# Kernel optimization log

Measured on AMD Instinct MI355X. Metric: run time of the kernel, lower is better.

Reference implementation:

```python
import jax, jax.numpy as jnp
import numpy as np

B, E, K = 512, 4096, 1024      # batch, emb_dim, key_dim
M, L = 1024, 32                # mem_size, prompt_length
TOP_K = 4
EPS = 1e-12


def _l2norm(x, axis=-1):
    n = jnp.linalg.norm(x, axis=axis, keepdims=True)
    return x / jnp.maximum(n, EPS)


def setup_inputs() -> dict:
    key = jax.random.key(0)
    k1, k2, k3, k4 = jax.random.split(key, 4)
    return {
        "x_query": jax.random.normal(k1, (B, E), dtype=jnp.float32),
        "W_proj": jax.random.normal(k2, (K, E), dtype=jnp.float32) * 0.02,
        "prompt_memory": jax.random.normal(k3, (M, L, E), dtype=jnp.float32) * 0.02,
        "prompt_keys": jax.random.normal(k4, (M, K), dtype=jnp.float32) * 0.02,
        "top_k": TOP_K,
    }


def reference(x_query, W_proj, prompt_memory, prompt_keys, top_k):
    # x_proj = Linear(emb_dim -> key_dim, no bias): x @ W.T
    x_proj = jnp.einsum("be,ke->bk", x_query, W_proj)          # [B, K]
    x_norm = _l2norm(x_proj)                                     # [B, K]
    key_norm = _l2norm(prompt_keys)                              # [M, K]
    sim = jnp.einsum("bk,mk->bm", x_norm, key_norm)             # [B, M]
    _, idx = jax.lax.top_k(sim, top_k)                           # [B, top_k]
    sel_prompts = prompt_memory[idx]                             # [B, top_k, L, E]
    sel_keys = _l2norm(prompt_keys[idx], axis=2)                 # [B, top_k, K]
    refined = jnp.einsum("bk,btk->bt", x_norm, sel_keys)        # [B, top_k]
    w = jax.nn.softmax(refined, axis=1)                          # [B, top_k]
    # softmax-weighted sum over selected prompts
    out = jnp.einsum("btle,bt->ble", sel_prompts, w)            # [B, L, E]
    return out
```

## Files before the change

kernel.cpp:

```cpp
#include <hip/hip_runtime.h>
#include <math.h>

#define BDIM 512
#define EDIM 4096
#define KDIM 1024
#define MDIM 1024
#define LDIM 32
#define TOPK 4
#define EPSF 1e-12f

typedef __attribute__((ext_vector_type(8))) short short8;
typedef __attribute__((ext_vector_type(4))) float f32x4;

struct us4 { ushort x, y, z, w; };

__device__ inline ushort f2bf_rn(float x) {
    union { float f; unsigned u; } v; v.f = x;
    unsigned r = (v.u + 0x7FFF + ((v.u >> 16) & 1)) >> 16;
    return (ushort)r;
}
__device__ inline float bf2f(ushort h) {
    union { unsigned u; float f; } v; v.u = ((unsigned)h) << 16;
    return v.f;
}

__global__ __launch_bounds__(256)
void split_all_kernel(const float* __restrict__ xq, const float* __restrict__ wp,
                      const float* __restrict__ pk,
                      ushort* __restrict__ xq_h, ushort* __restrict__ xq_l,
                      ushort* __restrict__ wp_h, ushort* __restrict__ wp_l,
                      ushort* __restrict__ pk_h, ushort* __restrict__ pk_l)
{
    const int blk = blockIdx.x;
    const float* src; ushort* hi; ushort* lo; int base;
    if (blk < 512)       { src = xq; hi = xq_h; lo = xq_l; base = blk * 1024; }
    else if (blk < 1536) { src = wp; hi = wp_h; lo = wp_l; base = (blk - 512) * 1024; }
    else                 { src = pk; hi = pk_h; lo = pk_l; base = (blk - 1536) * 1024; }

    #pragma unroll
    for (int it = 0; it < 4; ++it) {
        const int i = base + it * 256 + threadIdx.x;
        float4 v = ((const float4*)src)[i];
        us4 h, l;
        h.x = f2bf_rn(v.x); l.x = f2bf_rn(v.x - bf2f(h.x));
        h.y = f2bf_rn(v.y); l.y = f2bf_rn(v.y - bf2f(h.y));
        h.z = f2bf_rn(v.z); l.z = f2bf_rn(v.z - bf2f(h.z));
        h.w = f2bf_rn(v.w); l.w = f2bf_rn(v.w - bf2f(h.w));
        ((us4*)hi)[i] = h;
        ((us4*)lo)[i] = l;
    }
}

__global__ __launch_bounds__(256)
void gemm_mfma_split(const ushort* __restrict__ Ah, const ushort* __restrict__ Al,
                     const ushort* __restrict__ Bh, const ushort* __restrict__ Bl,
                     float* __restrict__ Cp, int M, int N, int K, int Kchunk)
{
    __shared__ ushort lds[4][64][40];

    const int t  = threadIdx.x;
    const int bn = blockIdx.x, bm = blockIdx.y, kz = blockIdx.z;

    const int srow = t >> 2, sg = t & 3;
    const size_t aoff = (size_t)(bm * 64 + srow) * K + sg * 8 + (size_t)kz * Kchunk;
    const size_t boff = (size_t)(bn * 64 + srow) * K + sg * 8 + (size_t)kz * Kchunk;

    const int lane = t & 63, wid = t >> 6;
    const int wr = wid >> 1, wc = wid & 1;
    const int fr = lane & 15, fg = lane >> 4;

    f32x4 acc[2][2];
    #pragma unroll
    for (int i = 0; i < 2; ++i)
        #pragma unroll
        for (int j = 0; j < 2; ++j)
            acc[i][j] = (f32x4){0.f, 0.f, 0.f, 0.f};

    for (int k0 = 0; k0 < Kchunk; k0 += 32) {
        *(short8*)(&lds[0][srow][sg * 8]) = *(const short8*)(Ah + aoff + k0);
        *(short8*)(&lds[1][srow][sg * 8]) = *(const short8*)(Al + aoff + k0);
        *(short8*)(&lds[2][srow][sg * 8]) = *(const short8*)(Bh + boff + k0);
        *(short8*)(&lds[3][srow][sg * 8]) = *(const short8*)(Bl + boff + k0);
        __syncthreads();

        short8 ah[2], al[2], bh[2], bl[2];
        #pragma unroll
        for (int i = 0; i < 2; ++i) {
            ah[i] = *(const short8*)(&lds[0][wr * 32 + i * 16 + fr][fg * 8]);
            al[i] = *(const short8*)(&lds[1][wr * 32 + i * 16 + fr][fg * 8]);
            bh[i] = *(const short8*)(&lds[2][wc * 32 + i * 16 + fr][fg * 8]);
            bl[i] = *(const short8*)(&lds[3][wc * 32 + i * 16 + fr][fg * 8]);
        }
        #pragma unroll
        for (int i = 0; i < 2; ++i)
            #pragma unroll
            for (int j = 0; j < 2; ++j) {
                acc[i][j] = __builtin_amdgcn_mfma_f32_16x16x32_bf16(ah[i], bh[j], acc[i][j], 0, 0, 0);
                acc[i][j] = __builtin_amdgcn_mfma_f32_16x16x32_bf16(ah[i], bl[j], acc[i][j], 0, 0, 0);
                acc[i][j] = __builtin_amdgcn_mfma_f32_16x16x32_bf16(al[i], bh[j], acc[i][j], 0, 0, 0);
            }
        __syncthreads();
    }

    float* Cz = Cp + (size_t)kz * M * N;
    #pragma unroll
    for (int i = 0; i < 2; ++i)
        #pragma unroll
        for (int j = 0; j < 2; ++j)
            #pragma unroll
            for (int q = 0; q < 4; ++q) {
                int orow = bm * 64 + wr * 32 + i * 16 + (lane >> 4) * 4 + q;
                int ocol = bn * 64 + wc * 32 + j * 16 + (lane & 15);
                Cz[(size_t)orow * N + ocol] = acc[i][j][q];
            }
}

__global__ __launch_bounds__(256)
void reduce_split_norm_kernel(const float* __restrict__ Cp,
                              ushort* __restrict__ xh, ushort* __restrict__ xl,
                              float* __restrict__ xn)
{
    const int b = blockIdx.x;
    const int i = b * 256 + threadIdx.x;
    const int n4 = BDIM * KDIM / 4;

    float4 s = ((const float4*)Cp)[i];
    #pragma unroll
    for (int z = 1; z < 4; ++z) {
        float4 v = ((const float4*)Cp)[(size_t)z * n4 + i];
        s.x += v.x; s.y += v.y; s.z += v.z; s.w += v.w;
    }

    us4 h, l;
    h.x = f2bf_rn(s.x); l.x = f2bf_rn(s.x - bf2f(h.x));
    h.y = f2bf_rn(s.y); l.y = f2bf_rn(s.y - bf2f(h.y));
    h.z = f2bf_rn(s.z); l.z = f2bf_rn(s.z - bf2f(h.z));
    h.w = f2bf_rn(s.w); l.w = f2bf_rn(s.w - bf2f(h.w));
    ((us4*)xh)[i] = h;
    ((us4*)xl)[i] = l;

    float sq = s.x * s.x + s.y * s.y + s.z * s.z + s.w * s.w;
    #pragma unroll
    for (int off = 32; off > 0; off >>= 1) sq += __shfl_down(sq, off, 64);
    __shared__ float wsum[4];
    const int lane = threadIdx.x & 63, wwid = threadIdx.x >> 6;
    if (lane == 0) wsum[wwid] = sq;
    __syncthreads();
    if (threadIdx.x == 0)
        xn[b] = sqrtf(wsum[0] + wsum[1] + wsum[2] + wsum[3]);
}

__global__ __launch_bounds__(256)
void reduce_scale_kernel(const float* __restrict__ Cp, const float* __restrict__ xn,
                         const float* __restrict__ kn, float* __restrict__ sim, int n4)
{
    int i = blockIdx.x * 256 + threadIdx.x;
    if (i >= n4) return;
    float4 s = ((const float4*)Cp)[i];
    float4 v = ((const float4*)Cp)[(size_t)n4 + i];
    s.x += v.x; s.y += v.y; s.z += v.z; s.w += v.w;
    const int b  = i >> 8;
    const int m0 = (i * 4) & 1023;
    const float sb = 1.f / fmaxf(xn[b], EPSF);
    s.x = s.x * sb / fmaxf(kn[m0 + 0], EPSF);
    s.y = s.y * sb / fmaxf(kn[m0 + 1], EPSF);
    s.z = s.z * sb / fmaxf(kn[m0 + 2], EPSF);
    s.w = s.w * sb / fmaxf(kn[m0 + 3], EPSF);
    ((float4*)sim)[i] = s;
}

__global__ __launch_bounds__(256)
void rownorm_kernel(const float* __restrict__ X, float* __restrict__ out, int ncols)
{
    const int row = blockIdx.x;
    const float* p = X + (size_t)row * ncols;
    float s = 0.f;
    for (int c = threadIdx.x * 4; c < ncols; c += 256 * 4) {
        float4 v = *(const float4*)(p + c);
        s += v.x * v.x + v.y * v.y + v.z * v.z + v.w * v.w;
    }
    #pragma unroll
    for (int off = 32; off > 0; off >>= 1) s += __shfl_down(s, off, 64);
    __shared__ float wsum[4];
    const int lane = threadIdx.x & 63, wwid = threadIdx.x >> 6;
    if (lane == 0) wsum[wwid] = s;
    __syncthreads();
    if (threadIdx.x == 0)
        out[row] = sqrtf(wsum[0] + wsum[1] + wsum[2] + wsum[3]);
}

__device__ inline bool tk_better(float x, int ix, float y, int iy) {
    return (x > y) || (x == y && ix < iy);
}
__device__ inline void tk_insert(float (&v)[4], int (&id)[4], float x, int m) {
    if (tk_better(x, m, v[3], id[3])) {
        v[3] = x; id[3] = m;
        if (tk_better(v[3], id[3], v[2], id[2])) {
            float tv = v[2]; int ti = id[2]; v[2] = v[3]; id[2] = id[3]; v[3] = tv; id[3] = ti;
            if (tk_better(v[2], id[2], v[1], id[1])) {
                tv = v[1]; ti = id[1]; v[1] = v[2]; id[1] = id[2]; v[2] = tv; id[2] = ti;
                if (tk_better(v[1], id[1], v[0], id[0])) {
                    tv = v[0]; ti = id[0]; v[0] = v[1]; id[0] = id[1]; v[1] = tv; id[1] = ti;
                }
            }
        }
    }
}
__global__ __launch_bounds__(64)
void topk_kernel(const float* __restrict__ sim, int* __restrict__ topi,
                 float* __restrict__ topv)
{
    const int b = blockIdx.x;
    const int lane = threadIdx.x;
    const float* row = sim + (size_t)b * MDIM;
    float v[4] = {-INFINITY, -INFINITY, -INFINITY, -INFINITY};
    int id[4] = {-1, -1, -1, -1};
    for (int j = 0; j < MDIM / 64; ++j) {
        int m = j * 64 + lane;
        tk_insert(v, id, row[m], m);
    }
    for (int off = 32; off >= 1; off >>= 1) {
        float pv[4]; int pi[4];
        #pragma unroll
        for (int q = 0; q < 4; ++q) {
            pv[q] = __shfl_xor(v[q], off, 64);
            pi[q] = __shfl_xor(id[q], off, 64);
        }
        #pragma unroll
        for (int q = 0; q < 4; ++q) tk_insert(v, id, pv[q], pi[q]);
    }
    if (lane == 0) {
        #pragma unroll
        for (int q = 0; q < 4; ++q) { topv[b * 4 + q] = v[q]; topi[b * 4 + q] = id[q]; }
    }
}

__global__ __launch_bounds__(256)
void gather_out_kernel(const float* __restrict__ pm, const int* __restrict__ topi,
                       const float* __restrict__ topv, float* __restrict__ out)
{
    const int bl = blockIdx.x;
    const int b = bl & (BDIM - 1);
    const int l = bl >> 9;

    const int j0 = topi[b * 4 + 0], j1 = topi[b * 4 + 1], j2 = topi[b * 4 + 2], j3 = topi[b * 4 + 3];
    const float r0 = topv[b * 4 + 0], r1 = topv[b * 4 + 1], r2 = topv[b * 4 + 2], r3 = topv[b * 4 + 3];
    const float mx = fmaxf(fmaxf(r0, r1), fmaxf(r2, r3));
    const float e0 = expf(r0 - mx), e1 = expf(r1 - mx), e2 = expf(r2 - mx), e3 = expf(r3 - mx);
    const float inv = 1.f / (e0 + e1 + e2 + e3);
    const float w0 = e0 * inv, w1 = e1 * inv, w2 = e2 * inv, w3 = e3 * inv;

    const f32x4* p0 = (const f32x4*)(pm + ((size_t)j0 * LDIM + l) * EDIM);
    const f32x4* p1 = (const f32x4*)(pm + ((size_t)j1 * LDIM + l) * EDIM);
    const f32x4* p2 = (const f32x4*)(pm + ((size_t)j2 * LDIM + l) * EDIM);
    const f32x4* p3 = (const f32x4*)(pm + ((size_t)j3 * LDIM + l) * EDIM);
    f32x4* o = (f32x4*)(out + ((size_t)b * LDIM + l) * EDIM);

    for (int c = threadIdx.x; c < EDIM / 4; c += 256) {
        f32x4 a = p0[c], bb = p1[c], cc = p2[c], dd = p3[c];
        f32x4 r = w0 * a + w1 * bb + w2 * cc + w3 * dd;
        __builtin_nontemporal_store(r, &o[c]);
    }
}

extern "C" void kernel_launch(void* const* d_in, const int* in_sizes, int n_in,
                              void* d_out, int out_size, void* d_ws, size_t ws_size,
                              hipStream_t stream)
{
    const float* x_query = (const float*)d_in[0];
    const float* W_proj  = (const float*)d_in[1];
    const float* pm      = (const float*)d_in[2];
    const float* pkeys   = (const float*)d_in[3];
    float* out = (float*)d_out;

    char* w = (char*)d_ws;
    ushort* xq_h = (ushort*)w; w += (size_t)BDIM * EDIM * 2;
    ushort* xq_l = (ushort*)w; w += (size_t)BDIM * EDIM * 2;
    ushort* wp_h = (ushort*)w; w += (size_t)KDIM * EDIM * 2;
    ushort* wp_l = (ushort*)w; w += (size_t)KDIM * EDIM * 2;
    ushort* pk_h = (ushort*)w; w += (size_t)MDIM * KDIM * 2;
    ushort* pk_l = (ushort*)w; w += (size_t)MDIM * KDIM * 2;
    ushort* xp_h = (ushort*)w; w += (size_t)BDIM * KDIM * 2;
    ushort* xp_l = (ushort*)w; w += (size_t)BDIM * KDIM * 2;
    float* Cp1    = (float*)w; w += (size_t)4 * BDIM * KDIM * 4;
    float* Cp2    = (float*)w; w += (size_t)2 * BDIM * MDIM * 4;
    float* sim    = (float*)w; w += (size_t)BDIM * MDIM * 4;
    float* xn     = (float*)w; w += BDIM * 4;
    float* kn     = (float*)w; w += MDIM * 4;
    float* topv   = (float*)w; w += BDIM * TOPK * 4;
    int*   topi   = (int*)w;   w += BDIM * TOPK * 4;

    split_all_kernel<<<1792, 256, 0, stream>>>(
        x_query, W_proj, pkeys, xq_h, xq_l, wp_h, wp_l, pk_h, pk_l);
    rownorm_kernel<<<MDIM, 256, 0, stream>>>(pkeys, kn, KDIM);

    gemm_mfma_split<<<dim3(KDIM / 64, BDIM / 64, 4), 256, 0, stream>>>(
        xq_h, xq_l, wp_h, wp_l, Cp1, BDIM, KDIM, EDIM, EDIM / 4);

    reduce_split_norm_kernel<<<BDIM, 256, 0, stream>>>(Cp1, xp_h, xp_l, xn);

    gemm_mfma_split<<<dim3(MDIM / 64, BDIM / 64, 2), 256, 0, stream>>>(
        xp_h, xp_l, pk_h, pk_l, Cp2, BDIM, MDIM, KDIM, KDIM / 2);
    reduce_scale_kernel<<<BDIM * MDIM / 4 / 256, 256, 0, stream>>>(
        Cp2, xn, kn, sim, BDIM * MDIM / 4);

    topk_kernel<<<BDIM, 64, 0, stream>>>(sim, topi, topv);

    gather_out_kernel<<<BDIM * LDIM, 256, 0, stream>>>(pm, topi, topv, out);
}
```

Before: 241.3 us.

## Fuse key norms into split, fuse scale into top-k, prefetch GEMM tiles

Computes the prompt-key row norms inside the bf16 split kernel, which removes the separate rownorm launch. Folds the split-K partial-sum reduction and cosine scaling into the top-k kernel, so the sim buffer and the reduce_scale launch are no longer needed. Adds register prefetch of the next K tile in the MFMA GEMM so global loads overlap with compute. The cost is extra barriers in the split blocks that handle prompt keys, plus more registers in the GEMM.

Result: no change. 240.3 us (-0.4%).

```diff
diff --git a/kernel.cpp b/kernel.cpp
--- a/kernel.cpp
+++ b/kernel.cpp
@@ -29,17 +29,24 @@
                       const float* __restrict__ pk,
                       ushort* __restrict__ xq_h, ushort* __restrict__ xq_l,
                       ushort* __restrict__ wp_h, ushort* __restrict__ wp_l,
-                      ushort* __restrict__ pk_h, ushort* __restrict__ pk_l)
+                      ushort* __restrict__ pk_h, ushort* __restrict__ pk_l,
+                      float* __restrict__ kn)
 {
     const int blk = blockIdx.x;
+    const int t = threadIdx.x;
     const float* src; ushort* hi; ushort* lo; int base;
+    bool do_norm = false; int rowbase = 0;
     if (blk < 512)       { src = xq; hi = xq_h; lo = xq_l; base = blk * 1024; }
     else if (blk < 1536) { src = wp; hi = wp_h; lo = wp_l; base = (blk - 512) * 1024; }
-    else                 { src = pk; hi = pk_h; lo = pk_l; base = (blk - 1536) * 1024; }
+    else                 { src = pk; hi = pk_h; lo = pk_l; base = (blk - 1536) * 1024;
+                           do_norm = true; rowbase = (blk - 1536) * 4; }
+
+    __shared__ float wsum[4];
+    const int lane = t & 63, wwid = t >> 6;
 
     #pragma unroll
     for (int it = 0; it < 4; ++it) {
-        const int i = base + it * 256 + threadIdx.x;
+        const int i = base + it * 256 + t;
         float4 v = ((const float4*)src)[i];
         us4 h, l;
         h.x = f2bf_rn(v.x); l.x = f2bf_rn(v.x - bf2f(h.x));
@@ -48,6 +55,17 @@
         h.w = f2bf_rn(v.w); l.w = f2bf_rn(v.w - bf2f(h.w));
         ((us4*)hi)[i] = h;
         ((us4*)lo)[i] = l;
+
+        if (do_norm) {
+            float sq = v.x * v.x + v.y * v.y + v.z * v.z + v.w * v.w;
+            #pragma unroll
+            for (int off = 32; off > 0; off >>= 1) sq += __shfl_down(sq, off, 64);
+            __syncthreads();
+            if (lane == 0) wsum[wwid] = sq;
+            __syncthreads();
+            if (t == 0)
+                kn[rowbase + it] = sqrtf(wsum[0] + wsum[1] + wsum[2] + wsum[3]);
+        }
     }
 }
 
@@ -76,12 +94,24 @@
         for (int j = 0; j < 2; ++j)
             acc[i][j] = (f32x4){0.f, 0.f, 0.f, 0.f};
 
+    short8 pA0 = *(const short8*)(Ah + aoff);
+    short8 pA1 = *(const short8*)(Al + aoff);
+    short8 pB0 = *(const short8*)(Bh + boff);
+    short8 pB1 = *(const short8*)(Bl + boff);
+
     for (int k0 = 0; k0 < Kchunk; k0 += 32) {
-        *(short8*)(&lds[0][srow][sg * 8]) = *(const short8*)(Ah + aoff + k0);
-        *(short8*)(&lds[1][srow][sg * 8]) = *(const short8*)(Al + aoff + k0);
-        *(short8*)(&lds[2][srow][sg * 8]) = *(const short8*)(Bh + boff + k0);
-        *(short8*)(&lds[3][srow][sg * 8]) = *(const short8*)(Bl + boff + k0);
+        *(short8*)(&lds[0][srow][sg * 8]) = pA0;
+        *(short8*)(&lds[1][srow][sg * 8]) = pA1;
+        *(short8*)(&lds[2][srow][sg * 8]) = pB0;
+        *(short8*)(&lds[3][srow][sg * 8]) = pB1;
         __syncthreads();
+
+        if (k0 + 32 < Kchunk) {
+            pA0 = *(const short8*)(Ah + aoff + k0 + 32);
+            pA1 = *(const short8*)(Al + aoff + k0 + 32);
+            pB0 = *(const short8*)(Bh + boff + k0 + 32);
+            pB1 = *(const short8*)(Bl + boff + k0 + 32);
+        }
 
         short8 ah[2], al[2], bh[2], bl[2];
         #pragma unroll
@@ -148,45 +178,6 @@
     __syncthreads();
     if (threadIdx.x == 0)
         xn[b] = sqrtf(wsum[0] + wsum[1] + wsum[2] + wsum[3]);
-}
-
-__global__ __launch_bounds__(256)
-void reduce_scale_kernel(const float* __restrict__ Cp, const float* __restrict__ xn,
-                         const float* __restrict__ kn, float* __restrict__ sim, int n4)
-{
-    int i = blockIdx.x * 256 + threadIdx.x;
-    if (i >= n4) return;
-    float4 s = ((const float4*)Cp)[i];
-    float4 v = ((const float4*)Cp)[(size_t)n4 + i];
-    s.x += v.x; s.y += v.y; s.z += v.z; s.w += v.w;
-    const int b  = i >> 8;
-    const int m0 = (i * 4) & 1023;
-    const float sb = 1.f / fmaxf(xn[b], EPSF);
-    s.x = s.x * sb / fmaxf(kn[m0 + 0], EPSF);
-    s.y = s.y * sb / fmaxf(kn[m0 + 1], EPSF);
-    s.z = s.z * sb / fmaxf(kn[m0 + 2], EPSF);
-    s.w = s.w * sb / fmaxf(kn[m0 + 3], EPSF);
-    ((float4*)sim)[i] = s;
-}
-
-__global__ __launch_bounds__(256)
-void rownorm_kernel(const float* __restrict__ X, float* __restrict__ out, int ncols)
-{
-    const int row = blockIdx.x;
-    const float* p = X + (size_t)row * ncols;
-    float s = 0.f;
-    for (int c = threadIdx.x * 4; c < ncols; c += 256 * 4) {
-        float4 v = *(const float4*)(p + c);
-        s += v.x * v.x + v.y * v.y + v.z * v.z + v.w * v.w;
-    }
-    #pragma unroll
-    for (int off = 32; off > 0; off >>= 1) s += __shfl_down(s, off, 64);
-    __shared__ float wsum[4];
-    const int lane = threadIdx.x & 63, wwid = threadIdx.x >> 6;
-    if (lane == 0) wsum[wwid] = s;
-    __syncthreads();
-    if (threadIdx.x == 0)
-        out[row] = sqrtf(wsum[0] + wsum[1] + wsum[2] + wsum[3]);
 }
 
 __device__ inline bool tk_better(float x, int ix, float y, int iy) {
@@ -207,17 +198,22 @@
     }
 }
 __global__ __launch_bounds__(64)
-void topk_kernel(const float* __restrict__ sim, int* __restrict__ topi,
-                 float* __restrict__ topv)
+void topk_scale_kernel(const float* __restrict__ Cp2, const float* __restrict__ xn,
+                       const float* __restrict__ kn,
+                       int* __restrict__ topi, float* __restrict__ topv)
 {
     const int b = blockIdx.x;
     const int lane = threadIdx.x;
-    const float* row = sim + (size_t)b * MDIM;
+    const float sb = 1.f / fmaxf(xn[b], EPSF);
+    const float* r0 = Cp2 + (size_t)b * MDIM;
+    const float* r1 = Cp2 + (size_t)BDIM * MDIM + (size_t)b * MDIM;
+
     float v[4] = {-INFINITY, -INFINITY, -INFINITY, -INFINITY};
     int id[4] = {-1, -1, -1, -1};
     for (int j = 0; j < MDIM / 64; ++j) {
         int m = j * 64 + lane;
-        tk_insert(v, id, row[m], m);
+        float s = (r0[m] + r1[m]) * sb / fmaxf(kn[m], EPSF);
+        tk_insert(v, id, s, m);
     }
     for (int off = 32; off >= 1; off >>= 1) {
         float pv[4]; int pi[4];
@@ -284,15 +280,13 @@
     ushort* xp_l = (ushort*)w; w += (size_t)BDIM * KDIM * 2;
     float* Cp1    = (float*)w; w += (size_t)4 * BDIM * KDIM * 4;
     float* Cp2    = (float*)w; w += (size_t)2 * BDIM * MDIM * 4;
-    float* sim    = (float*)w; w += (size_t)BDIM * MDIM * 4;
     float* xn     = (float*)w; w += BDIM * 4;
     float* kn     = (float*)w; w += MDIM * 4;
     float* topv   = (float*)w; w += BDIM * TOPK * 4;
     int*   topi   = (int*)w;   w += BDIM * TOPK * 4;
 
     split_all_kernel<<<1792, 256, 0, stream>>>(
-        x_query, W_proj, pkeys, xq_h, xq_l, wp_h, wp_l, pk_h, pk_l);
-    rownorm_kernel<<<MDIM, 256, 0, stream>>>(pkeys, kn, KDIM);
+        x_query, W_proj, pkeys, xq_h, xq_l, wp_h, wp_l, pk_h, pk_l, kn);
 
     gemm_mfma_split<<<dim3(KDIM / 64, BDIM / 64, 4), 256, 0, stream>>>(
         xq_h, xq_l, wp_h, wp_l, Cp1, BDIM, KDIM, EDIM, EDIM / 4);
@@ -301,10 +295,8 @@
 
     gemm_mfma_split<<<dim3(MDIM / 64, BDIM / 64, 2), 256, 0, stream>>>(
         xp_h, xp_l, pk_h, pk_l, Cp2, BDIM, MDIM, KDIM, KDIM / 2);
-    reduce_scale_kernel<<<BDIM * MDIM / 4 / 256, 256, 0, stream>>>(
-        Cp2, xn, kn, sim, BDIM * MDIM / 4);
-
-    topk_kernel<<<BDIM, 64, 0, stream>>>(sim, topi, topv);
+
+    topk_scale_kernel<<<BDIM, 64, 0, stream>>>(Cp2, xn, kn, topi, topv);
 
     gather_out_kernel<<<BDIM * LDIM, 256, 0, stream>>>(pm, topi, topv, out);
 }
```
